# Kernel tuning notes

Measured on AMD Instinct MI355X. Metric: run time of the kernel, lower is better.

The kernel has to match this reference:

```python
import jax, jax.numpy as jnp
import numpy as np

LENGTH = 320  # hard-coded in the layer
BIG = 1e5     # cap for 'no zero pixel in column' distances; BIG**2 = 1e10 -> exp() underflows to 0


def _edt_sq(zero):
    """Exact squared Euclidean distance transform.

    zero: [N, H, W] bool, True where the uint8-restored mask is 0 (seed pixels).
    Returns [N, H, W] float32 squared distance of every pixel to the nearest seed.
    Phase 1: 1D distance along H via associative scans (nearest seed above/below).
    Phase 2: exact lower envelope over W via a vectorized min-reduction:
             D2[n,i,j] = min_x ( (j-x)^2 + g2[n,i,x] ).
    """
    N, H, W = zero.shape
    ih = jnp.arange(H, dtype=jnp.float32)[None, :, None]            # [1,H,1]
    last = jax.lax.associative_scan(jnp.maximum,
                                    jnp.where(zero, ih, -BIG), axis=1)
    nxt = jax.lax.associative_scan(jnp.minimum,
                                   jnp.where(zero, ih, 2.0 * BIG), axis=1,
                                   reverse=True)
    g = jnp.minimum(jnp.minimum(ih - last, nxt - ih), BIG)           # [N,H,W] 1D dist
    g2 = g * g
    jw = jnp.arange(W, dtype=jnp.float32)
    off = (jw[:, None] - jw[None, :]) ** 2                           # [Wj, Wx]
    # [N,H,Wj,Wx] broadcast + min over source column x
    d2 = jnp.min(g2[:, :, None, :] + off[None, None], axis=-1)
    return d2


def _forward(inputs):
    B, H, W, _ = inputs.shape
    # uint8 cast: zero iff (1-x)*127.5 < 1  (matches tf.cast truncation)
    restored = ((1.0 - jax.lax.stop_gradient(inputs)) * 127.5).astype(jnp.uint8)
    zero = restored == 0                                             # [B,H,W,2]
    zm = jnp.moveaxis(zero, -1, 1).reshape(B * 2, H, W)              # fold channel into batch
    d2 = _edt_sq(zm).reshape(B, 2, H, W)
    sigmas = jnp.asarray([0.02, 0.08, 0.16], jnp.float32) * LENGTH   # [3]
    denom = 2.0 * sigmas * sigmas
    # exp(-d^2 / (2 sigma^2)) for each (channel, sigma); channel-major order like the loop
    clicks = jnp.exp(-d2[:, :, None] / denom[None, None, :, None, None])  # [B,2,3,H,W]
    return jnp.moveaxis(clicks.reshape(B, 6, H, W), 1, -1)          # [B,H,W,6]


def setup_inputs() -> dict:
    key = jax.random.key(0)
    inputs = jax.random.uniform(key, (4, 320, 320, 2), dtype=jnp.float32)
    return {"inputs": inputs}


def reference(inputs):
    return _forward(inputs)
```

## Files before the change

### kernel.cpp

```cpp
#include <hip/hip_runtime.h>

#define HH 320
#define WW 320
#define NIMG 8
#define BIGF 1.0e5f

#define TW  16
#define NCH 32
#define CH  10

__global__ __launch_bounds__(512) void edt_vert(const float* __restrict__ in,
                                                float* __restrict__ g2) {
    int wl = threadIdx.x;
    int ch = threadIdx.y;
    int b  = blockIdx.x / 20;
    int wt = blockIdx.x % 20;
    int w  = wt * TW + wl;
    int h0 = ch * CH;

    const float2* ip = (const float2*)in + (size_t)(b * HH + h0) * WW + w;
    float2 v[CH];
    #pragma unroll
    for (int k = 0; k < CH; ++k) v[k] = ip[(size_t)k * WW];

    unsigned m0 = 0, m1 = 0;
    #pragma unroll
    for (int k = 0; k < CH; ++k) {
        if ((1.0f - v[k].x) * 127.5f < 1.0f) m0 |= 1u << k;
        if ((1.0f - v[k].y) * 127.5f < 1.0f) m1 |= 1u << k;
    }

    __shared__ float sL[2][NCH][TW], sN[2][NCH][TW];
    sL[0][ch][wl] = m0 ? (float)(h0 + 31 - __clz((int)m0)) : -1.0e9f;
    sL[1][ch][wl] = m1 ? (float)(h0 + 31 - __clz((int)m1)) : -1.0e9f;
    sN[0][ch][wl] = m0 ? (float)(h0 + __ffs((int)m0) - 1)  :  1.0e9f;
    sN[1][ch][wl] = m1 ? (float)(h0 + __ffs((int)m1) - 1)  :  1.0e9f;
    __syncthreads();

    float L0 = -1.0e9f, L1 = -1.0e9f, N0 = 1.0e9f, N1 = 1.0e9f;
    for (int cc = 0; cc < NCH; ++cc) {
        float a0 = sL[0][cc][wl], a1 = sL[1][cc][wl];
        float b0 = sN[0][cc][wl], b1 = sN[1][cc][wl];
        if (cc < ch) { L0 = fmaxf(L0, a0); L1 = fmaxf(L1, a1); }
        if (cc > ch) { N0 = fminf(N0, b0); N1 = fminf(N1, b1); }
    }

    float gd0[CH], gd1[CH];
    float r0 = L0, r1 = L1;
    #pragma unroll
    for (int k = 0; k < CH; ++k) {
        float fh = (float)(h0 + k);
        if (m0 & (1u << k)) r0 = fh;
        if (m1 & (1u << k)) r1 = fh;
        gd0[k] = fh - r0;
        gd1[k] = fh - r1;
    }
    float* gp0 = g2 + ((size_t)(b * 2 + 0) * HH + h0) * WW + w;
    float* gp1 = g2 + ((size_t)(b * 2 + 1) * HH + h0) * WW + w;
    r0 = N0; r1 = N1;
    #pragma unroll
    for (int k = CH - 1; k >= 0; --k) {
        float fh = (float)(h0 + k);
        if (m0 & (1u << k)) r0 = fh;
        if (m1 & (1u << k)) r1 = fh;
        float g0 = fminf(fminf(gd0[k], r0 - fh), BIGF);
        float g1 = fminf(fminf(gd1[k], r1 - fh), BIGF);
        gp0[(size_t)k * WW] = g0 * g0;
        gp1[(size_t)k * WW] = g1 * g1;
    }
}

__global__ __launch_bounds__(256) void edt_horiz(const float* __restrict__ g2,
                                                 float* __restrict__ out) {
    int wv   = threadIdx.x >> 6;
    int lane = threadIdx.x & 63;
    int b  = blockIdx.x / 160;
    int hp = blockIdx.x % 160;
    int hh = wv >> 1;
    int c  = wv & 1;
    int row = (2 * b + c) * HH + (2 * hp + hh);

    __shared__ __align__(16) float sa[4][WW];
    __shared__ float sd2[2][2][WW];

    const float* grow = g2 + (size_t)row * WW;
    #pragma unroll
    for (int m = 0; m < 5; ++m) {
        int x = lane + 64 * m;
        float fx = (float)x;
        sa[wv][x] = fmaf(fx, fx, grow[x]);
    }

    const float4* sv = (const float4*)sa[wv];
    float d2v[5], n2j[5];
    #pragma unroll
    for (int m = 0; m < 5; ++m) {
        d2v[m] = 3.4e38f;
        n2j[m] = -2.0f * (float)(lane + 64 * m);
    }

    float4 cur[8], nxt[8];
    #pragma unroll
    for (int q = 0; q < 8; ++q) cur[q] = sv[q];
    #pragma unroll
    for (int t = 0; t < 10; ++t) {
        if (t < 9) {
            #pragma unroll
            for (int q = 0; q < 8; ++q) nxt[q] = sv[8 * (t + 1) + q];
        }
        #pragma unroll
        for (int q = 0; q < 8; ++q) {
            float a0 = cur[q].x, a1 = cur[q].y, a2 = cur[q].z, a3 = cur[q].w;
            float x0 = (float)(32 * t + 4 * q);
            #pragma unroll
            for (int m = 0; m < 5; ++m) {
                float t0 = fmaf(n2j[m], x0,        a0);
                float t1 = fmaf(n2j[m], x0 + 1.0f, a1);
                float t2 = fmaf(n2j[m], x0 + 2.0f, a2);
                float t3 = fmaf(n2j[m], x0 + 3.0f, a3);
                d2v[m] = fminf(fminf(d2v[m], fminf(t0, t1)), fminf(t2, t3));
            }
        }
        #pragma unroll
        for (int q = 0; q < 8; ++q) cur[q] = nxt[q];
    }

    #pragma unroll
    for (int m = 0; m < 5; ++m) {
        float fj = (float)(lane + 64 * m);
        sd2[hh][c][lane + 64 * m] = fmaf(fj, fj, d2v[m]);
    }
    __syncthreads();

    float* obase = out + (size_t)(b * HH + 2 * hp) * WW * 6;
    for (int q = threadIdx.x; q < 960; q += 256) {
        int D = 4 * q;
        int hh2 = D / 1920;
        int rr = D - 1920 * hh2;
        float vals[4];
        #pragma unroll
        for (int e = 0; e < 4; ++e) {
            int idx = rr + e;
            int jj = idx / 6;
            int cs = idx - 6 * jj;
            int c2 = (cs >= 3) ? 1 : 0;
            int s  = cs - 3 * c2;
            float dd = sd2[hh2][c2][jj];
            float co = (s == 0) ? (1.0f / 81.92f)
                     : (s == 1) ? (1.0f / 1310.72f)
                                : (1.0f / 5242.88f);
            vals[e] = __expf(-dd * co);
        }
        float4 o = {vals[0], vals[1], vals[2], vals[3]};
        *(float4*)(obase + D) = o;
    }
}

extern "C" void kernel_launch(void* const* d_in, const int* in_sizes, int n_in,
                              void* d_out, int out_size, void* d_ws, size_t ws_size,
                              hipStream_t stream) {
    const float* in = (const float*)d_in[0];
    float* out = (float*)d_out;
    float* g2 = (float*)d_ws;

    edt_vert<<<4 * 20, dim3(TW, NCH), 0, stream>>>(in, g2);
    edt_horiz<<<4 * 160, 256, 0, stream>>>(g2, out);
}
```

Before: 74.11 us.

## Fuse vertical and horizontal EDT passes into one cooperative kernel with grid sync

```diff
diff --git a/kernel.cpp b/kernel.cpp
--- a/kernel.cpp
+++ b/kernel.cpp
@@ -1,158 +1,165 @@
 #include <hip/hip_runtime.h>
+#include <hip/hip_cooperative_groups.h>
+
+namespace cg = cooperative_groups;
 
 #define HH 320
 #define WW 320
-#define NIMG 8
 #define BIGF 1.0e5f
 
-#define TW  16
-#define NCH 32
-#define CH  10
+__global__ __launch_bounds__(256) void edt_fused(const float* __restrict__ in,
+                                                 float* __restrict__ g2,
+                                                 float* __restrict__ out) {
+    cg::grid_group grid = cg::this_grid();
+    const int tid = threadIdx.x;
+    const int blk = blockIdx.x;
 
-__global__ __launch_bounds__(512) void edt_vert(const float* __restrict__ in,
-                                                float* __restrict__ g2) {
-    int wl = threadIdx.x;
-    int ch = threadIdx.y;
-    int b  = blockIdx.x / 20;
-    int wt = blockIdx.x % 20;
-    int w  = wt * TW + wl;
-    int h0 = ch * CH;
-
-    const float2* ip = (const float2*)in + (size_t)(b * HH + h0) * WW + w;
-    float2 v[CH];
-    #pragma unroll
-    for (int k = 0; k < CH; ++k) v[k] = ip[(size_t)k * WW];
-
-    unsigned m0 = 0, m1 = 0;
-    #pragma unroll
-    for (int k = 0; k < CH; ++k) {
-        if ((1.0f - v[k].x) * 127.5f < 1.0f) m0 |= 1u << k;
-        if ((1.0f - v[k].y) * 127.5f < 1.0f) m1 |= 1u << k;
-    }
-
-    __shared__ float sL[2][NCH][TW], sN[2][NCH][TW];
-    sL[0][ch][wl] = m0 ? (float)(h0 + 31 - __clz((int)m0)) : -1.0e9f;
-    sL[1][ch][wl] = m1 ? (float)(h0 + 31 - __clz((int)m1)) : -1.0e9f;
-    sN[0][ch][wl] = m0 ? (float)(h0 + __ffs((int)m0) - 1)  :  1.0e9f;
-    sN[1][ch][wl] = m1 ? (float)(h0 + __ffs((int)m1) - 1)  :  1.0e9f;
-    __syncthreads();
-
-    float L0 = -1.0e9f, L1 = -1.0e9f, N0 = 1.0e9f, N1 = 1.0e9f;
-    for (int cc = 0; cc < NCH; ++cc) {
-        float a0 = sL[0][cc][wl], a1 = sL[1][cc][wl];
-        float b0 = sN[0][cc][wl], b1 = sN[1][cc][wl];
-        if (cc < ch) { L0 = fmaxf(L0, a0); L1 = fmaxf(L1, a1); }
-        if (cc > ch) { N0 = fminf(N0, b0); N1 = fminf(N1, b1); }
-    }
-
-    float gd0[CH], gd1[CH];
-    float r0 = L0, r1 = L1;
-    #pragma unroll
-    for (int k = 0; k < CH; ++k) {
-        float fh = (float)(h0 + k);
-        if (m0 & (1u << k)) r0 = fh;
-        if (m1 & (1u << k)) r1 = fh;
-        gd0[k] = fh - r0;
-        gd1[k] = fh - r1;
-    }
-    float* gp0 = g2 + ((size_t)(b * 2 + 0) * HH + h0) * WW + w;
-    float* gp1 = g2 + ((size_t)(b * 2 + 1) * HH + h0) * WW + w;
-    r0 = N0; r1 = N1;
-    #pragma unroll
-    for (int k = CH - 1; k >= 0; --k) {
-        float fh = (float)(h0 + k);
-        if (m0 & (1u << k)) r0 = fh;
-        if (m1 & (1u << k)) r1 = fh;
-        float g0 = fminf(fminf(gd0[k], r0 - fh), BIGF);
-        float g1 = fminf(fminf(gd1[k], r1 - fh), BIGF);
-        gp0[(size_t)k * WW] = g0 * g0;
-        gp1[(size_t)k * WW] = g1 * g1;
-    }
-}
-
-__global__ __launch_bounds__(256) void edt_horiz(const float* __restrict__ g2,
-                                                 float* __restrict__ out) {
-    int wv   = threadIdx.x >> 6;
-    int lane = threadIdx.x & 63;
-    int b  = blockIdx.x / 160;
-    int hp = blockIdx.x % 160;
-    int hh = wv >> 1;
-    int c  = wv & 1;
-    int row = (2 * b + c) * HH + (2 * hp + hh);
-
+    __shared__ float sL[2][32][8], sN[2][32][8];
     __shared__ __align__(16) float sa[4][WW];
     __shared__ float sd2[2][2][WW];
 
-    const float* grow = g2 + (size_t)row * WW;
-    #pragma unroll
-    for (int m = 0; m < 5; ++m) {
-        int x = lane + 64 * m;
-        float fx = (float)x;
-        sa[wv][x] = fmaf(fx, fx, grow[x]);
+    if (blk < 160) {
+        int wl = tid & 7;
+        int ch = tid >> 3;
+        int b  = blk / 40;
+        int wt = blk % 40;
+        int w  = wt * 8 + wl;
+        int h0 = ch * 10;
+
+        const float2* ip = (const float2*)in + (size_t)(b * HH + h0) * WW + w;
+        float2 v[10];
+        #pragma unroll
+        for (int k = 0; k < 10; ++k) v[k] = ip[(size_t)k * WW];
+
+        unsigned m0 = 0, m1 = 0;
+        #pragma unroll
+        for (int k = 0; k < 10; ++k) {
+            if ((1.0f - v[k].x) * 127.5f < 1.0f) m0 |= 1u << k;
+            if ((1.0f - v[k].y) * 127.5f < 1.0f) m1 |= 1u << k;
+        }
+
+        sL[0][ch][wl] = m0 ? (float)(h0 + 31 - __clz((int)m0)) : -1.0e9f;
+        sL[1][ch][wl] = m1 ? (float)(h0 + 31 - __clz((int)m1)) : -1.0e9f;
+        sN[0][ch][wl] = m0 ? (float)(h0 + __ffs((int)m0) - 1)  :  1.0e9f;
+        sN[1][ch][wl] = m1 ? (float)(h0 + __ffs((int)m1) - 1)  :  1.0e9f;
+        __syncthreads();
+
+        float L0 = -1.0e9f, L1 = -1.0e9f, N0 = 1.0e9f, N1 = 1.0e9f;
+        for (int cc = 0; cc < 32; ++cc) {
+            float a0 = sL[0][cc][wl], a1 = sL[1][cc][wl];
+            float b0 = sN[0][cc][wl], b1 = sN[1][cc][wl];
+            if (cc < ch) { L0 = fmaxf(L0, a0); L1 = fmaxf(L1, a1); }
+            if (cc > ch) { N0 = fminf(N0, b0); N1 = fminf(N1, b1); }
+        }
+
+        float gd0[10], gd1[10];
+        float r0 = L0, r1 = L1;
+        #pragma unroll
+        for (int k = 0; k < 10; ++k) {
+            float fh = (float)(h0 + k);
+            if (m0 & (1u << k)) r0 = fh;
+            if (m1 & (1u << k)) r1 = fh;
+            gd0[k] = fh - r0;
+            gd1[k] = fh - r1;
+        }
+        float* gp0 = g2 + ((size_t)(b * 2 + 0) * HH + h0) * WW + w;
+        float* gp1 = g2 + ((size_t)(b * 2 + 1) * HH + h0) * WW + w;
+        r0 = N0; r1 = N1;
+        #pragma unroll
+        for (int k = 9; k >= 0; --k) {
+            float fh = (float)(h0 + k);
+            if (m0 & (1u << k)) r0 = fh;
+            if (m1 & (1u << k)) r1 = fh;
+            float g0 = fminf(fminf(gd0[k], r0 - fh), BIGF);
+            float g1 = fminf(fminf(gd1[k], r1 - fh), BIGF);
+            gp0[(size_t)k * WW] = g0 * g0;
+            gp1[(size_t)k * WW] = g1 * g1;
+        }
     }
 
-    const float4* sv = (const float4*)sa[wv];
-    float d2v[5], n2j[5];
-    #pragma unroll
-    for (int m = 0; m < 5; ++m) {
-        d2v[m] = 3.4e38f;
-        n2j[m] = -2.0f * (float)(lane + 64 * m);
-    }
+    __threadfence();
+    grid.sync();
 
-    float4 cur[8], nxt[8];
-    #pragma unroll
-    for (int q = 0; q < 8; ++q) cur[q] = sv[q];
-    #pragma unroll
-    for (int t = 0; t < 10; ++t) {
-        if (t < 9) {
+    {
+        int wv   = tid >> 6;
+        int lane = tid & 63;
+        int b  = blk / 160;
+        int hp = blk % 160;
+        int hh = wv >> 1;
+        int c  = wv & 1;
+        int row = (2 * b + c) * HH + (2 * hp + hh);
+
+        const float* grow = g2 + (size_t)row * WW;
+        #pragma unroll
+        for (int m = 0; m < 5; ++m) {
+            int x = lane + 64 * m;
+            float fx = (float)x;
+            sa[wv][x] = fmaf(fx, fx, grow[x]);
+        }
+
+        const float4* sv = (const float4*)sa[wv];
+        float d2v[5], n2j[5];
+        #pragma unroll
+        for (int m = 0; m < 5; ++m) {
+            d2v[m] = 3.4e38f;
+            n2j[m] = -2.0f * (float)(lane + 64 * m);
+        }
+
+        float4 cur[8], nxt[8];
+        #pragma unroll
+        for (int q = 0; q < 8; ++q) cur[q] = sv[q];
+        #pragma unroll
+        for (int t = 0; t < 10; ++t) {
+            if (t < 9) {
+                #pragma unroll
+                for (int q = 0; q < 8; ++q) nxt[q] = sv[8 * (t + 1) + q];
+            }
             #pragma unroll
-            for (int q = 0; q < 8; ++q) nxt[q] = sv[8 * (t + 1) + q];
+            for (int q = 0; q < 8; ++q) {
+                float a0 = cur[q].x, a1 = cur[q].y, a2 = cur[q].z, a3 = cur[q].w;
+                float x0 = (float)(32 * t + 4 * q);
+                #pragma unroll
+                for (int m = 0; m < 5; ++m) {
+                    float t0 = fmaf(n2j[m], x0,        a0);
+                    float t1 = fmaf(n2j[m], x0 + 1.0f, a1);
+                    float t2 = fmaf(n2j[m], x0 + 2.0f, a2);
+                    float t3 = fmaf(n2j[m], x0 + 3.0f, a3);
+                    d2v[m] = fminf(fminf(d2v[m], fminf(t0, t1)), fminf(t2, t3));
+                }
+            }
+            #pragma unroll
+            for (int q = 0; q < 8; ++q) cur[q] = nxt[q];
         }
+
         #pragma unroll
-        for (int q = 0; q < 8; ++q) {
-            float a0 = cur[q].x, a1 = cur[q].y, a2 = cur[q].z, a3 = cur[q].w;
-            float x0 = (float)(32 * t + 4 * q);
+        for (int m = 0; m < 5; ++m) {
+            float fj = (float)(lane + 64 * m);
+            sd2[hh][c][lane + 64 * m] = fmaf(fj, fj, d2v[m]);
+        }
+        __syncthreads();
+
+        float* obase = out + (size_t)(b * HH + 2 * hp) * WW * 6;
+        for (int q = tid; q < 960; q += 256) {
+            int D = 4 * q;
+            int hh2 = D / 1920;
+            int rr = D - 1920 * hh2;
+            float vals[4];
             #pragma unroll
-            for (int m = 0; m < 5; ++m) {
-                float t0 = fmaf(n2j[m], x0,        a0);
-                float t1 = fmaf(n2j[m], x0 + 1.0f, a1);
-                float t2 = fmaf(n2j[m], x0 + 2.0f, a2);
-                float t3 = fmaf(n2j[m], x0 + 3.0f, a3);
-                d2v[m] = fminf(fminf(d2v[m], fminf(t0, t1)), fminf(t2, t3));
+            for (int e = 0; e < 4; ++e) {
+                int idx = rr + e;
+                int jj = idx / 6;
+                int cs = idx - 6 * jj;
+                int c2 = (cs >= 3) ? 1 : 0;
+                int s  = cs - 3 * c2;
+                float dd = sd2[hh2][c2][jj];
+                float co = (s == 0) ? (1.0f / 81.92f)
+                         : (s == 1) ? (1.0f / 1310.72f)
+                                    : (1.0f / 5242.88f);
+                vals[e] = __expf(-dd * co);
             }
+            float4 o = {vals[0], vals[1], vals[2], vals[3]};
+            *(float4*)(obase + D) = o;
         }
-        #pragma unroll
-        for (int q = 0; q < 8; ++q) cur[q] = nxt[q];
-    }
-
-    #pragma unroll
-    for (int m = 0; m < 5; ++m) {
-        float fj = (float)(lane + 64 * m);
-        sd2[hh][c][lane + 64 * m] = fmaf(fj, fj, d2v[m]);
-    }
-    __syncthreads();
-
-    float* obase = out + (size_t)(b * HH + 2 * hp) * WW * 6;
-    for (int q = threadIdx.x; q < 960; q += 256) {
-        int D = 4 * q;
-        int hh2 = D / 1920;
-        int rr = D - 1920 * hh2;
-        float vals[4];
-        #pragma unroll
-        for (int e = 0; e < 4; ++e) {
-            int idx = rr + e;
-            int jj = idx / 6;
-            int cs = idx - 6 * jj;
-            int c2 = (cs >= 3) ? 1 : 0;
-            int s  = cs - 3 * c2;
-            float dd = sd2[hh2][c2][jj];
-            float co = (s == 0) ? (1.0f / 81.92f)
-                     : (s == 1) ? (1.0f / 1310.72f)
-                                : (1.0f / 5242.88f);
-            vals[e] = __expf(-dd * co);
-        }
-        float4 o = {vals[0], vals[1], vals[2], vals[3]};
-        *(float4*)(obase + D) = o;
     }
 }
 
@@ -163,6 +170,7 @@
     float* out = (float*)d_out;
     float* g2 = (float*)d_ws;
 
-    edt_vert<<<4 * 20, dim3(TW, NCH), 0, stream>>>(in, g2);
-    edt_horiz<<<4 * 160, 256, 0, stream>>>(g2, out);
+    void* args[] = {(void*)&in, (void*)&g2, (void*)&out};
+    hipLaunchCooperativeKernel((void*)edt_fused, dim3(640), dim3(256),
+                               args, 0, stream);
 }
```

New measurement: 216.2 us. 192% more time.
